# Kernel optimization log

Measured on AMD Instinct MI355X. Metric: run time of the kernel, lower is better.

## Reference

```python
import jax, jax.numpy as jnp
import numpy as np

N = 50000
E = 800000
F_IN = 128
HID = 64
HEADS = 4
N_LAYERS = 3
EDGE_DIM = 9
NEG_SLOPE_ATT = 0.2   # GATv2Conv attention leaky_relu slope
NEG_SLOPE_OUT = 0.01  # F.leaky_relu default between layers


def _glorot(key, shape):
    fan_in, fan_out = shape[0], shape[1]
    lim = jnp.sqrt(6.0 / (fan_in + fan_out))
    return jax.random.uniform(key, shape, jnp.float32, -lim, lim)


def setup_inputs() -> dict:
    key = jax.random.key(0)
    ks = jax.random.split(key, 20)
    HC = HEADS * HID
    L = N_LAYERS - 1
    inp = {
        "x": jax.random.normal(ks[0], (N, F_IN), jnp.float32),
        "edge_attr": jax.random.normal(ks[1], (E, EDGE_DIM), jnp.float32),
        # init conv params (in = F_IN)
        "init_Wl": _glorot(ks[2], (F_IN, HC)),
        "init_bl": jnp.full((HC,), 0.01, jnp.float32),
        "init_Wr": _glorot(ks[3], (F_IN, HC)),
        "init_br": jnp.full((HC,), 0.01, jnp.float32),
        "init_We": _glorot(ks[4], (EDGE_DIM, HC)),
        "init_att": _glorot(ks[5], (HEADS, HID)),
        "init_bias": jnp.zeros((HID,), jnp.float32),
        # stacked params for remaining layers (in = HID)
        "Wl": jax.vmap(lambda k: _glorot(k, (HID, HC)))(jax.random.split(ks[6], L)),
        "bl": jnp.full((L, HC), 0.01, jnp.float32),
        "Wr": jax.vmap(lambda k: _glorot(k, (HID, HC)))(jax.random.split(ks[7], L)),
        "br": jnp.full((L, HC), 0.01, jnp.float32),
        "We": jax.vmap(lambda k: _glorot(k, (EDGE_DIM, HC)))(jax.random.split(ks[8], L)),
        "att": jax.vmap(lambda k: _glorot(k, (HEADS, HID)))(jax.random.split(ks[9], L)),
        "bias": jnp.zeros((L, HID), jnp.float32),
        "gates": jax.random.normal(ks[10], (N_LAYERS,), jnp.float32),
        "edge_index": jax.random.randint(ks[11], (2, E), 0, N, jnp.int32).astype(jnp.int64),
    }
    return inp


def gatv2_layer(x, src, dst, edge_attr, Wl, bl, Wr, br, We, att, bias):
    n = x.shape[0]
    xl = (x @ Wl + bl).reshape(n, HEADS, HID)   # source transform
    xr = (x @ Wr + br).reshape(n, HEADS, HID)   # target transform
    e = (edge_attr @ We).reshape(-1, HEADS, HID)
    m = xl[src] + xr[dst] + e                   # [E, H, C]
    s = jax.nn.leaky_relu(m, NEG_SLOPE_ATT)
    logits = jnp.einsum('ehc,hc->eh', s, att)   # [E, H]
    # per-destination segment softmax (stable)
    mx = jax.ops.segment_max(logits, dst, num_segments=n)
    mx = jnp.where(jnp.isfinite(mx), mx, 0.0)
    p = jnp.exp(logits - mx[dst])
    denom = jax.ops.segment_sum(p, dst, num_segments=n)
    alpha = p / (denom[dst] + 1e-16)
    msg = xl[src] * alpha[..., None]            # [E, H, C]
    out = jax.ops.segment_sum(msg, dst, num_segments=n)  # [N, H, C]
    return out.mean(axis=1) + bias              # concat=False -> head mean


def reference(x, edge_index, edge_attr, init_Wl, init_bl, init_Wr, init_br,
              init_We, init_att, init_bias, Wl, bl, Wr, br, We, att, bias, gates):
    src, dst = edge_index[0], edge_index[1]
    g = jax.nn.sigmoid(gates)
    h = gatv2_layer(x, src, dst, edge_attr, init_Wl, init_bl, init_Wr, init_br,
                    init_We, init_att, init_bias)
    for i in range(N_LAYERS - 1):
        h = jax.nn.leaky_relu(h, NEG_SLOPE_OUT)
        h_new = gatv2_layer(h, src, dst, edge_attr, Wl[i], bl[i], Wr[i], br[i],
                            We[i], att[i], bias[i])
        h = g[i] * h_new + (1.0 - g[i]) * h
    return h
```

## Files before the change

kernel.cpp:

```cpp
#include <hip/hip_runtime.h>
#include <hip/hip_fp16.h>
#include <math.h>

#define N_NODES 50000
#define N_EDGES 800000
#define F_IN    128
#define HID     64
#define HEADS   4
#define HC      256
#define HC2     512
#define EDIM    9
#define EDUP    20
#define NSCAN   ((N_NODES + 255) / 256)

typedef float v2f __attribute__((ext_vector_type(2)));
typedef float f32x4 __attribute__((ext_vector_type(4)));
typedef _Float16 half8 __attribute__((ext_vector_type(8)));

__device__ inline v2f cvt2(unsigned int u) {
    const __half2 h = __builtin_bit_cast(__half2, u);
    const float2 f = __half22float2(h);
    return (v2f){f.x, f.y};
}

__global__ void convert_x(const float* __restrict__ in, _Float16* __restrict__ out, int n8) {
    const int i = blockIdx.x * 256 + threadIdx.x;
    if (i >= n8) return;
    const float4 f0 = *(const float4*)(in + (size_t)i * 8);
    const float4 f1 = *(const float4*)(in + (size_t)i * 8 + 4);
    half8 o;
    o[0] = (_Float16)f0.x; o[1] = (_Float16)f0.y; o[2] = (_Float16)f0.z; o[3] = (_Float16)f0.w;
    o[4] = (_Float16)f1.x; o[5] = (_Float16)f1.y; o[6] = (_Float16)f1.z; o[7] = (_Float16)f1.w;
    *(half8*)(out + (size_t)i * 8) = o;
}

template<int K>
__global__ void pack_w(const float* __restrict__ Wl, const float* __restrict__ Wr,
                       const float* __restrict__ bl, const float* __restrict__ br,
                       _Float16* __restrict__ Wp, float* __restrict__ biascat) {
    constexpr int KS = K / 32;
    const int tid = blockIdx.x * 256 + threadIdx.x;
    if (tid < HC2) biascat[tid] = (tid < HC) ? bl[tid] : br[tid - HC];
    if (tid >= 32 * KS * 64) return;
    const int l = tid & 63;
    const int rest = tid >> 6;
    const int ks = rest % KS;
    const int ct = rest / KS;
    const int col = ct * 16 + (l & 15);
    const int kb = ks * 32 + (l >> 4) * 8;
    half8 o;
    #pragma unroll
    for (int j = 0; j < 8; ++j) {
        const int k = kb + j;
        const float v = (col < HC) ? Wl[(size_t)k * HC + col] : Wr[(size_t)k * HC + col - HC];
        o[j] = (_Float16)v;
    }
    *(half8*)(Wp + (size_t)tid * 8) = o;
}

template<int K>
__global__ __launch_bounds__(256) void nt_mfma(
        const _Float16* __restrict__ xin, const _Float16* __restrict__ Wp,
        const float* __restrict__ biascat, __half* __restrict__ xlr) {
    constexpr int KS = K / 32;
    const int mt = blockIdx.x * 4 + (threadIdx.x >> 6);
    if (mt >= N_NODES / 16) return;
    const int lane = threadIdx.x & 63;
    const int l15 = lane & 15;
    const int kg = lane >> 4;

    half8 a[KS];
    #pragma unroll
    for (int ks = 0; ks < KS; ++ks)
        a[ks] = *(const half8*)(xin + (size_t)(mt * 16 + l15) * K + ks * 32 + kg * 8);

    const half8* __restrict__ Wp8 = (const half8*)Wp;
    #pragma unroll 2
    for (int ct = 0; ct < 32; ++ct) {
        f32x4 d = {0.f, 0.f, 0.f, 0.f};
        #pragma unroll
        for (int ks = 0; ks < KS; ++ks)
            d = __builtin_amdgcn_mfma_f32_16x16x32_f16(a[ks], Wp8[(size_t)(ct * KS + ks) * 64 + lane], d, 0, 0, 0);
        const float bc = biascat[ct * 16 + l15];
        #pragma unroll
        for (int r = 0; r < 4; ++r) {
            const int node = mt * 16 + kg * 4 + r;
            xlr[(size_t)node * HC2 + ct * 16 + l15] = __float2half(d[r] + bc);
        }
    }
}

__global__ void zero_counts(int* __restrict__ counts, int* __restrict__ cursor) {
    const int i = blockIdx.x * blockDim.x + threadIdx.x;
    if (i < N_NODES) { counts[i] = 0; cursor[i] = 0; }
}

__global__ void count_deg(const int* __restrict__ dst, int* __restrict__ counts) {
    const int e = blockIdx.x * blockDim.x + threadIdx.x;
    if (e < N_EDGES) atomicAdd(&counts[dst[e]], 1);
}

__global__ void scanA(const int* __restrict__ counts, int* __restrict__ bsum) {
    __shared__ int s[256];
    const int t = threadIdx.x;
    const int i = blockIdx.x * 256 + t;
    s[t] = (i < N_NODES) ? counts[i] : 0;
    __syncthreads();
    for (int st = 128; st > 0; st >>= 1) {
        if (t < st) s[t] += s[t + st];
        __syncthreads();
    }
    if (t == 0) bsum[blockIdx.x] = s[0];
}

__global__ void scanB(const int* __restrict__ bsum, int* __restrict__ boff) {
    __shared__ int s[256];
    const int t = threadIdx.x;
    const int orig = (t < NSCAN) ? bsum[t] : 0;
    s[t] = orig;
    __syncthreads();
    for (int st = 1; st < 256; st <<= 1) {
        int v = (t >= st) ? s[t - st] : 0;
        __syncthreads();
        s[t] += v;
        __syncthreads();
    }
    if (t < NSCAN) boff[t] = s[t] - orig;
}

__global__ void scanC(const int* __restrict__ counts, const int* __restrict__ boff,
                      int* __restrict__ offs) {
    __shared__ int s[256];
    const int t = threadIdx.x;
    const int i = blockIdx.x * 256 + t;
    const int orig = (i < N_NODES) ? counts[i] : 0;
    s[t] = orig;
    __syncthreads();
    for (int st = 1; st < 256; st <<= 1) {
        int v = (t >= st) ? s[t - st] : 0;
        __syncthreads();
        s[t] += v;
        __syncthreads();
    }
    if (i < N_NODES) offs[i] = boff[blockIdx.x] + s[t] - orig;
    if (i == 0) offs[N_NODES] = N_EDGES;
}

__global__ void fill_csr(const int* __restrict__ src, const int* __restrict__ dst,
                         const int* __restrict__ offs, int* __restrict__ cursor,
                         const float* __restrict__ ea,
                         int* __restrict__ srcp, int* __restrict__ perm,
                         float* __restrict__ eap, int permuted) {
    const int e = blockIdx.x * blockDim.x + threadIdx.x;
    if (e >= N_EDGES) return;
    const int d = dst[e];
    const int pos = offs[d] + atomicAdd(&cursor[d], 1);
    srcp[pos] = src[e];
    perm[pos] = e;
    if (permuted) {
        float v[EDUP];
        #pragma unroll
        for (int u = 0; u < EDIM; ++u) {
            const float ev = ea[(size_t)e * EDIM + u];
            v[2 * u] = ev; v[2 * u + 1] = ev;
        }
        v[18] = 0.f; v[19] = 0.f;
        float4* o = (float4*)(eap + (size_t)pos * EDUP);
        #pragma unroll
        for (int u = 0; u < 5; ++u) o[u] = *(float4*)(v + 4 * u);
    }
}

template<int PERMUTED>
__global__ __launch_bounds__(64) void fused_edge(
        const __half* __restrict__ xlr,
        const float* __restrict__ eap, const float* __restrict__ ea,
        const int* __restrict__ perm,
        const int* __restrict__ offs, const int* __restrict__ srcp,
        const float* __restrict__ We, const float* __restrict__ att,
        const float* __restrict__ bias, const float* __restrict__ gates,
        float* __restrict__ h, __half* __restrict__ hact, int layer) {
    const int d = blockIdx.x;
    const int lane = threadIdx.x;
    const int c0 = lane * 4;

    v2f vxr01, vxr23;
    {
        const uint2 raw = *(const uint2*)(xlr + (size_t)d * HC2 + HC + c0);
        vxr01 = cvt2(raw.x); vxr23 = cvt2(raw.y);
    }
    const float4 wa4 = *(const float4*)(att + c0);
    const float wa0 = wa4.x * 1.44269504f, wa1 = wa4.y * 1.44269504f,
                wa2 = wa4.z * 1.44269504f, wa3 = wa4.w * 1.44269504f;
    v2f wWe01[EDIM], wWe23[EDIM];
    #pragma unroll
    for (int u = 0; u < EDIM; ++u) {
        const float4 w4 = *(const float4*)(We + u * HC + c0);
        wWe01[u] = (v2f){w4.x, w4.y};
        wWe23[u] = (v2f){w4.z, w4.w};
    }
    const v2f c02 = (v2f){0.2f, 0.2f};

    float den = 0.f;
    v2f acc01 = (v2f){0.f, 0.f}, acc23 = (v2f){0.f, 0.f};

    const int jb = offs[d], je = offs[d + 1];

    uint2 rawA, rawB;
    v2f eA[EDIM], eB[EDIM];

    auto loadE = [&](int j, uint2& raw, v2f (&ef)[EDIM]) {
        const int s = srcp[j];
        raw = *(const uint2*)(xlr + (size_t)s * HC2 + c0);
        if (PERMUTED) {
            const v2f* ep = (const v2f*)(eap + (size_t)j * EDUP);
            #pragma unroll
            for (int u = 0; u < EDIM; ++u) ef[u] = ep[u];
        } else {
            const float* ep = ea + (size_t)perm[j] * EDIM;
            #pragma unroll
            for (int u = 0; u < EDIM; ++u) { const float ev = ep[u]; ef[u] = (v2f){ev, ev}; }
        }
    };

    auto compute = [&](const uint2 raw, const v2f (&ef)[EDIM]) {
        const v2f a01 = cvt2(raw.x), a23 = cvt2(raw.y);
        v2f m01 = a01 + vxr01;
        v2f m23 = a23 + vxr23;
        #pragma unroll
        for (int u = 0; u < EDIM; ++u) {
            m01 = __builtin_elementwise_fma(ef[u], wWe01[u], m01);
            m23 = __builtin_elementwise_fma(ef[u], wWe23[u], m23);
        }
        const v2f s01 = __builtin_elementwise_max(m01, m01 * c02);
        const v2f s23 = __builtin_elementwise_max(m23, m23 * c02);
        float l = fmaf(s01.x, wa0, fmaf(s01.y, wa1, fmaf(s23.x, wa2, s23.y * wa3)));
        l += __shfl_xor(l, 1, 64);
        l += __shfl_xor(l, 2, 64);
        l += __shfl_xor(l, 4, 64);
        l += __shfl_xor(l, 8, 64);
        const float p = __builtin_amdgcn_exp2f(fminf(l, 108.f));
        den += p;
        const v2f pp = (v2f){p, p};
        acc01 = __builtin_elementwise_fma(pp, a01, acc01);
        acc23 = __builtin_elementwise_fma(pp, a23, acc23);
    };

    int j = jb;
    if (j < je) loadE(j, rawA, eA);
    while (j + 1 < je) {
        loadE(j + 1, rawB, eB);
        compute(rawA, eA);
        if (j + 2 < je) {
            loadE(j + 2, rawA, eA);
            compute(rawB, eB);
        } else {
            compute(rawB, eB);
        }
        j += 2;
    }
    if (j < je) compute(rawA, eA);

    const float inv = 1.f / (den + 1e-16f);
    float4 v;
    v.x = acc01.x * inv; v.y = acc01.y * inv; v.z = acc23.x * inv; v.w = acc23.y * inv;
    v.x += __shfl_xor(v.x, 16, 64);  v.x += __shfl_xor(v.x, 32, 64);
    v.y += __shfl_xor(v.y, 16, 64);  v.y += __shfl_xor(v.y, 32, 64);
    v.z += __shfl_xor(v.z, 16, 64);  v.z += __shfl_xor(v.z, 32, 64);
    v.w += __shfl_xor(v.w, 16, 64);  v.w += __shfl_xor(v.w, 32, 64);

    if (lane < 16) {
        const int c = lane * 4;
        float4 outv;
        outv.x = fmaf(0.25f, v.x, bias[c + 0]);
        outv.y = fmaf(0.25f, v.y, bias[c + 1]);
        outv.z = fmaf(0.25f, v.z, bias[c + 2]);
        outv.w = fmaf(0.25f, v.w, bias[c + 3]);
        if (layer > 0) {
            const float g = 1.f / (1.f + __expf(-gates[layer - 1]));
            float4 pv = *(const float4*)(h + (size_t)d * HID + c);
            pv.x = fmaxf(pv.x, 0.01f * pv.x);
            pv.y = fmaxf(pv.y, 0.01f * pv.y);
            pv.z = fmaxf(pv.z, 0.01f * pv.z);
            pv.w = fmaxf(pv.w, 0.01f * pv.w);
            outv.x = g * outv.x + (1.f - g) * pv.x;
            outv.y = g * outv.y + (1.f - g) * pv.y;
            outv.z = g * outv.z + (1.f - g) * pv.z;
            outv.w = g * outv.w + (1.f - g) * pv.w;
        }
        *(float4*)(h + (size_t)d * HID + c) = outv;
        if (layer < 2) {
            const __half2 p01 = __floats2half2_rn(fmaxf(outv.x, 0.01f * outv.x),
                                                  fmaxf(outv.y, 0.01f * outv.y));
            const __half2 p23 = __floats2half2_rn(fmaxf(outv.z, 0.01f * outv.z),
                                                  fmaxf(outv.w, 0.01f * outv.w));
            uint2 o;
            o.x = __builtin_bit_cast(unsigned int, p01);
            o.y = __builtin_bit_cast(unsigned int, p23);
            *(uint2*)(hact + (size_t)d * HID + c) = o;
        }
    }
}

extern "C" void kernel_launch(void* const* d_in, const int* in_sizes, int n_in,
                              void* d_out, int out_size, void* d_ws, size_t ws_size,
                              hipStream_t stream) {
    const float* x     = (const float*)d_in[0];
    const float* ea    = (const float*)d_in[1];
    const float* iWl   = (const float*)d_in[2];
    const float* ibl   = (const float*)d_in[3];
    const float* iWr   = (const float*)d_in[4];
    const float* ibr   = (const float*)d_in[5];
    const float* iWe   = (const float*)d_in[6];
    const float* iatt  = (const float*)d_in[7];
    const float* ibias = (const float*)d_in[8];
    const float* Wl    = (const float*)d_in[9];
    const float* bl    = (const float*)d_in[10];
    const float* Wr    = (const float*)d_in[11];
    const float* br    = (const float*)d_in[12];
    const float* We    = (const float*)d_in[13];
    const float* att   = (const float*)d_in[14];
    const float* bias  = (const float*)d_in[15];
    const float* gates = (const float*)d_in[16];
    const int*   ei    = (const int*)d_in[17];
    const int* src = ei;
    const int* dst = ei + N_EDGES;

    __half*    xlr     = (__half*)d_ws;
    __half*    hact    = xlr + (size_t)N_NODES * HC2;
    _Float16*  x16     = (_Float16*)(hact + (size_t)N_NODES * HID);
    _Float16*  Wp      = x16 + (size_t)N_NODES * F_IN;
    float*     biascat = (float*)(Wp + 512 * 128);
    int* counts = (int*)(biascat + HC2);
    int* cursor = counts + N_NODES;
    int* offs   = cursor + N_NODES;
    int* bsum   = offs + N_NODES + 1;
    int* boff   = bsum + 256;
    int* srcp   = boff + 256;
    int* perm   = srcp + N_EDGES;
    float* eap  = (float*)(((uintptr_t)(perm + N_EDGES) + 15) & ~(uintptr_t)15);
    float* h    = (float*)d_out;

    const size_t need = (size_t)((char*)(eap + (size_t)N_EDGES * EDUP) - (char*)d_ws);
    const int permuted = (ws_size >= need) ? 1 : 0;

    zero_counts<<<(N_NODES + 255) / 256, 256, 0, stream>>>(counts, cursor);
    count_deg<<<(N_EDGES + 255) / 256, 256, 0, stream>>>(dst, counts);
    scanA<<<NSCAN, 256, 0, stream>>>(counts, bsum);
    scanB<<<1, 256, 0, stream>>>(bsum, boff);
    scanC<<<NSCAN, 256, 0, stream>>>(counts, boff, offs);
    fill_csr<<<(N_EDGES + 255) / 256, 256, 0, stream>>>(src, dst, offs, cursor, ea,
                                                        srcp, perm, eap, permuted);
    convert_x<<<(N_NODES * F_IN / 8 + 255) / 256, 256, 0, stream>>>(x, x16, N_NODES * F_IN / 8);

    const int MT = N_NODES / 16;
    const int NTB = (MT + 3) / 4;

    for (int layer = 0; layer < 3; ++layer) {
        const float* wl_   = (layer == 0) ? iWl   : Wl   + (size_t)(layer - 1) * HID * HC;
        const float* bl_   = (layer == 0) ? ibl   : bl   + (size_t)(layer - 1) * HC;
        const float* wr_   = (layer == 0) ? iWr   : Wr   + (size_t)(layer - 1) * HID * HC;
        const float* br_   = (layer == 0) ? ibr   : br   + (size_t)(layer - 1) * HC;
        const float* we_   = (layer == 0) ? iWe   : We   + (size_t)(layer - 1) * EDIM * HC;
        const float* att_  = (layer == 0) ? iatt  : att  + (size_t)(layer - 1) * HC;
        const float* bias_ = (layer == 0) ? ibias : bias + (size_t)(layer - 1) * HID;

        if (layer == 0) {
            pack_w<F_IN><<<32, 256, 0, stream>>>(wl_, wr_, bl_, br_, Wp, biascat);
            nt_mfma<F_IN><<<NTB, 256, 0, stream>>>(x16, Wp, biascat, xlr);
        } else {
            pack_w<HID><<<16, 256, 0, stream>>>(wl_, wr_, bl_, br_, Wp, biascat);
            nt_mfma<HID><<<NTB, 256, 0, stream>>>((const _Float16*)hact, Wp, biascat, xlr);
        }

        if (permuted)
            fused_edge<1><<<N_NODES, 64, 0, stream>>>(xlr, eap, ea, perm, offs, srcp,
                                                      we_, att_, bias_, gates, h, hact, layer);
        else
            fused_edge<0><<<N_NODES, 64, 0, stream>>>(xlr, eap, ea, perm, offs, srcp,
                                                      we_, att_, bias_, gates, h, hact, layer);
    }
}
```

Baseline: 503.2 us.

## Sort destination nodes by degree and pack two nodes per edge block

Adds a degree histogram, prefix scan and scatter that produce a node ordering grouped by in-degree. The fused edge kernel now runs two 64-lane waves per 128-thread block, each handling one node taken from this ordering. This is meant to balance work across waves in a block and cut block scheduling overhead, at the cost of three extra small preprocessing kernels and less locality in output writes. Degrees are bucketed modulo 256, which only affects grouping, not correctness.

```diff
diff --git a/kernel.cpp b/kernel.cpp
--- a/kernel.cpp
+++ b/kernel.cpp
@@ -90,9 +90,11 @@
     }
 }
 
-__global__ void zero_counts(int* __restrict__ counts, int* __restrict__ cursor) {
+__global__ void zero_counts(int* __restrict__ counts, int* __restrict__ cursor,
+                            int* __restrict__ hist, int* __restrict__ hcur) {
     const int i = blockIdx.x * blockDim.x + threadIdx.x;
     if (i < N_NODES) { counts[i] = 0; cursor[i] = 0; }
+    if (blockIdx.x == 0 && threadIdx.x < 256) { hist[threadIdx.x] = 0; hcur[threadIdx.x] = 0; }
 }
 
 __global__ void count_deg(const int* __restrict__ dst, int* __restrict__ counts) {
@@ -144,6 +146,35 @@
     }
     if (i < N_NODES) offs[i] = boff[blockIdx.x] + s[t] - orig;
     if (i == 0) offs[N_NODES] = N_EDGES;
+}
+
+__global__ void hist_deg(const int* __restrict__ counts, int* __restrict__ hist) {
+    const int i = blockIdx.x * blockDim.x + threadIdx.x;
+    if (i < N_NODES) atomicAdd(&hist[counts[i] & 255], 1);
+}
+
+__global__ void scan_hist(const int* __restrict__ hist, int* __restrict__ hoff) {
+    __shared__ int s[256];
+    const int t = threadIdx.x;
+    const int orig = hist[t];
+    s[t] = orig;
+    __syncthreads();
+    for (int st = 1; st < 256; st <<= 1) {
+        int v = (t >= st) ? s[t - st] : 0;
+        __syncthreads();
+        s[t] += v;
+        __syncthreads();
+    }
+    hoff[t] = s[t] - orig;
+}
+
+__global__ void scatter_nodes(const int* __restrict__ counts, const int* __restrict__ hoff,
+                              int* __restrict__ hcur, int* __restrict__ order) {
+    const int i = blockIdx.x * blockDim.x + threadIdx.x;
+    if (i >= N_NODES) return;
+    const int deg = counts[i] & 255;
+    const int pos = hoff[deg] + atomicAdd(&hcur[deg], 1);
+    order[pos] = i;
 }
 
 __global__ void fill_csr(const int* __restrict__ src, const int* __restrict__ dst,
@@ -172,16 +203,16 @@
 }
 
 template<int PERMUTED>
-__global__ __launch_bounds__(64) void fused_edge(
+__global__ __launch_bounds__(128) void fused_edge(
         const __half* __restrict__ xlr,
         const float* __restrict__ eap, const float* __restrict__ ea,
-        const int* __restrict__ perm,
+        const int* __restrict__ perm, const int* __restrict__ order,
         const int* __restrict__ offs, const int* __restrict__ srcp,
         const float* __restrict__ We, const float* __restrict__ att,
         const float* __restrict__ bias, const float* __restrict__ gates,
         float* __restrict__ h, __half* __restrict__ hact, int layer) {
-    const int d = blockIdx.x;
-    const int lane = threadIdx.x;
+    const int d = __builtin_amdgcn_readfirstlane(order[blockIdx.x * 2 + (threadIdx.x >> 6)]);
+    const int lane = threadIdx.x & 63;
     const int c0 = lane * 4;
 
     v2f vxr01, vxr23;
@@ -336,19 +367,26 @@
     int* offs   = cursor + N_NODES;
     int* bsum   = offs + N_NODES + 1;
     int* boff   = bsum + 256;
-    int* srcp   = boff + 256;
+    int* hist   = boff + 256;
+    int* hoff   = hist + 256;
+    int* hcur   = hoff + 256;
+    int* srcp   = hcur + 256;
     int* perm   = srcp + N_EDGES;
-    float* eap  = (float*)(((uintptr_t)(perm + N_EDGES) + 15) & ~(uintptr_t)15);
+    int* order  = perm + N_EDGES;
+    float* eap  = (float*)(((uintptr_t)(order + N_NODES) + 15) & ~(uintptr_t)15);
     float* h    = (float*)d_out;
 
     const size_t need = (size_t)((char*)(eap + (size_t)N_EDGES * EDUP) - (char*)d_ws);
     const int permuted = (ws_size >= need) ? 1 : 0;
 
-    zero_counts<<<(N_NODES + 255) / 256, 256, 0, stream>>>(counts, cursor);
+    zero_counts<<<(N_NODES + 255) / 256, 256, 0, stream>>>(counts, cursor, hist, hcur);
     count_deg<<<(N_EDGES + 255) / 256, 256, 0, stream>>>(dst, counts);
     scanA<<<NSCAN, 256, 0, stream>>>(counts, bsum);
     scanB<<<1, 256, 0, stream>>>(bsum, boff);
     scanC<<<NSCAN, 256, 0, stream>>>(counts, boff, offs);
+    hist_deg<<<NSCAN, 256, 0, stream>>>(counts, hist);
+    scan_hist<<<1, 256, 0, stream>>>(hist, hoff);
+    scatter_nodes<<<NSCAN, 256, 0, stream>>>(counts, hoff, hcur, order);
     fill_csr<<<(N_EDGES + 255) / 256, 256, 0, stream>>>(src, dst, offs, cursor, ea,
                                                         srcp, perm, eap, permuted);
     convert_x<<<(N_NODES * F_IN / 8 + 255) / 256, 256, 0, stream>>>(x, x16, N_NODES * F_IN / 8);
@@ -374,10 +412,10 @@
         }
 
         if (permuted)
-            fused_edge<1><<<N_NODES, 64, 0, stream>>>(xlr, eap, ea, perm, offs, srcp,
-                                                      we_, att_, bias_, gates, h, hact, layer);
+            fused_edge<1><<<N_NODES / 2, 128, 0, stream>>>(xlr, eap, ea, perm, order, offs, srcp,
+                                                           we_, att_, bias_, gates, h, hact, layer);
         else
-            fused_edge<0><<<N_NODES, 64, 0, stream>>>(xlr, eap, ea, perm, offs, srcp,
-                                                      we_, att_, bias_, gates, h, hact, layer);
-    }
-}
+            fused_edge<0><<<N_NODES / 2, 128, 0, stream>>>(xlr, eap, ea, perm, order, offs, srcp,
+                                                           we_, att_, bias_, gates, h, hact, layer);
+    }
+}
```

Result: slower. 752.4 us (+49.5%).
